# Kernel optimization log

Measured on AMD Instinct MI355X. Metric: run time of the kernel, lower is better.

The kernel has to match this reference:

```python
import jax, jax.numpy as jnp
import numpy as np

K = 2  # shift stride from module init


def setup_inputs() -> dict:
    key = jax.random.key(0)
    k1, k2, k3 = jax.random.split(key, 3)
    # x: [B, C, D, H, W] dense volumetric features
    x = jax.random.normal(k1, (2, 128, 48, 48, 48), dtype=jnp.float32)
    # 1x1x1 Conv3d weight [out_channels, 2*in_channels] (kernel dims squeezed) + bias
    W = jax.random.normal(k2, (128, 256), dtype=jnp.float32) * 0.02
    b = jax.random.normal(k3, (128,), dtype=jnp.float32) * 0.02
    return {"x": x, "W": W, "b": b}


def _max_relative(x):
    # torch.cat([x[..., -i:], x[..., :-i]], dim=ax) == roll by +i along ax
    B, C, D, H, Wd = x.shape
    xj = jnp.zeros_like(x)  # x - x
    for axis, n in ((2, D), (3, H), (4, Wd)):
        for i in range(K, n, K):  # static shift schedule, fine under jit
            xj = jnp.maximum(xj, x - jnp.roll(x, i, axis=axis))
    return xj


def reference(x, W, b):
    xj = _max_relative(x)
    y = jnp.concatenate([x, xj], axis=1)  # [B, 2C, D, H, W]
    # 1x1x1 conv == channel GEMM
    out = jnp.einsum('bcdhw,oc->bodhw', y, W) + b[None, :, None, None, None]
    return jax.nn.relu(out)
```

## Files before the change

kernel.cpp:

```cpp
#include <hip/hip_runtime.h>
#include <hip/hip_bf16.h>

#define SVOL 110592
#define HD   2304
#define NDIM 48

typedef __attribute__((ext_vector_type(4))) float f32x4;
typedef __attribute__((ext_vector_type(8))) short bf16x8;
typedef __attribute__((ext_vector_type(2))) unsigned int u32x2;
typedef unsigned short ushort_t;
typedef unsigned int uint_t;

__global__ __launch_bounds__(256) void wconv_kernel(const float* __restrict__ W,
                                                    ushort_t* __restrict__ Wb) {
    int i = blockIdx.x * 256 + threadIdx.x;
    float f = W[i];
    __hip_bfloat16 h = __float2bfloat16(f);
    Wb[i] = *(ushort_t*)&h;
}

__global__ __launch_bounds__(256) void tables_kernel(const float* __restrict__ x,
                                                     float* __restrict__ tabDp,
                                                     float* __restrict__ tabH,
                                                     float* __restrict__ tabW) {
    __shared__ __align__(16) float sl[4 * HD];
    const int bc   = blockIdx.x;
    const int part = blockIdx.y;
    const float* __restrict__ xp = x + (size_t)bc * SVOL + (size_t)part * 16 * HD;
    const int t    = threadIdx.x;
    const int w4   = t >> 6;
    const int lane = t & 63;
    const int dlh  = t / NDIM;
    const int wh   = t - dlh * NDIM;

    f32x4 accD[3][2];
    #pragma unroll
    for (int s = 0; s < 3; ++s)
        #pragma unroll
        for (int p = 0; p < 2; ++p)
            #pragma unroll
            for (int e = 0; e < 4; ++e) accD[s][p][e] = 3e38f;

    for (int q = 0; q < 4; ++q) {
        const float* __restrict__ qp = xp + (size_t)q * 4 * HD;
        #pragma unroll
        for (int k = 0; k < 9; ++k) {
            const int i16 = (k * 4 + w4) * 64 + lane;
            __builtin_amdgcn_global_load_lds(
                (const __attribute__((address_space(1))) void*)(qp + (size_t)i16 * 4),
                (__attribute__((address_space(3))) void*)&sl[(k * 4 + w4) * 256],
                16, 0, 0);
        }
        __syncthreads();

        #pragma unroll
        for (int s = 0; s < 3; ++s) {
            const int j = t + s * 256;
            if (j < 576) {
                #pragma unroll
                for (int dl = 0; dl < 4; ++dl) {
                    f32x4 v = ((const f32x4*)sl)[dl * 576 + j];
                    #pragma unroll
                    for (int e = 0; e < 4; ++e)
                        accD[s][dl & 1][e] = fminf(accD[s][dl & 1][e], v[e]);
                }
            }
        }
        if (t < 192) {
            const int d = part * 16 + q * 4 + dlh;
            {
                const float* pb = sl + dlh * HD + wh;
                float m0 = 3e38f, m1 = 3e38f;
                #pragma unroll
                for (int h = 0; h < NDIM; h += 2) {
                    m0 = fminf(m0, pb[h * NDIM]);
                    m1 = fminf(m1, pb[(h + 1) * NDIM]);
                }
                tabH[(size_t)bc * 2 * HD + d * NDIM + wh]      = m0;
                tabH[(size_t)bc * 2 * HD + HD + d * NDIM + wh] = m1;
            }
            {
                const f32x4* pr = (const f32x4*)(sl + dlh * HD + wh * NDIM);
                const int rot = wh % 12;
                float m0 = 3e38f, m1 = 3e38f;
                #pragma unroll
                for (int j = 0; j < 12; ++j) {
                    int jj = j + rot; if (jj >= 12) jj -= 12;
                    f32x4 v = pr[jj];
                    m0 = fminf(m0, fminf(v[0], v[2]));
                    m1 = fminf(m1, fminf(v[1], v[3]));
                }
                tabW[(size_t)bc * 2 * HD + d * NDIM + wh]      = m0;
                tabW[(size_t)bc * 2 * HD + HD + d * NDIM + wh] = m1;
            }
        }
        __syncthreads();
    }

    float* tDo = tabDp + ((size_t)part * 256 + bc) * 2 * HD;
    #pragma unroll
    for (int s = 0; s < 3; ++s) {
        const int j = t + s * 256;
        if (j < 576) {
            *((f32x4*)(tDo + j * 4))      = accD[s][0];
            *((f32x4*)(tDo + HD + j * 4)) = accD[s][1];
        }
    }
}

__global__ __launch_bounds__(256) void merge_kernel(const float* __restrict__ tabDp,
                                                    float* __restrict__ tabD) {
    const int i = blockIdx.x * 256 + threadIdx.x;
    f32x4 a  = ((const f32x4*)tabDp)[i];
    f32x4 d1 = ((const f32x4*)(tabDp + (size_t)256 * 2 * HD))[i];
    f32x4 d2 = ((const f32x4*)(tabDp + (size_t)2 * 256 * 2 * HD))[i];
    f32x4 m;
    #pragma unroll
    for (int j = 0; j < 4; ++j) m[j] = fminf(a[j], fminf(d1[j], d2[j]));
    ((f32x4*)tabD)[i] = m;
}

#define TPB 4
__global__ __launch_bounds__(256, 2) void gemm_kernel(const float* __restrict__ x,
                                                      const float* __restrict__ tabD,
                                                      const float* __restrict__ tabH,
                                                      const float* __restrict__ tabW,
                                                      const ushort_t* __restrict__ Wb,
                                                      const float* __restrict__ bias,
                                                      float* __restrict__ out) {
    __shared__ __align__(1024) ushort_t ytile[16384];
    const int tile0 = blockIdx.x * TPB;
    const int b  = blockIdx.y;
    const int t  = threadIdx.x;
    const int wid = t >> 6, lane = t & 63;
    const int row  = lane & 3;
    const int colq = (lane >> 2) & 3;
    const int sqq  = (lane >> 4) & 3;
    const int sloc = (sqq * 4 + colq) * 4;
    const int l15 = lane & 15, l4 = lane >> 4;

    const float* __restrict__ xb = x + (size_t)b * 128 * SVOL;
    const size_t tbb = (size_t)b * 128 * 2 * HD;

    const ushort_t* wp = Wb + (size_t)(wid * 32 + l15) * 256 + l4 * 8;
    float bv[2];
    #pragma unroll
    for (int m = 0; m < 2; ++m) bv[m] = bias[wid * 32 + m * 16 + l15];

    const int d  = (tile0 * 64) / HD;
    const int rb = tile0 * 64 - d * HD;
    const int pd = d & 1;

    uint2 pk[8][2];
    auto stage = [&](int tile) {
        const int r  = rb + (tile - tile0) * 64 + sloc;
        const int h  = r / NDIM;
        const int w0 = r - h * NDIM;
        const int ph = h & 1;
        const int s  = d * HD + r;
        #pragma unroll
        for (int it = 0; it < 8; ++it) {
            const int c = (it * 4 + wid) * 4 + row;
            const size_t tb = tbb + (size_t)c * 2 * HD;
            f32x4 xv = *(const f32x4*)(xb + (size_t)c * SVOL + s);
            f32x4 mD = *(const f32x4*)(tabD + tb + pd * HD + r);
            f32x4 mH = *(const f32x4*)(tabH + tb + ph * HD + d * NDIM + w0);
            const float mW0 = tabW[tb + d * NDIM + h];
            const float mW1 = tabW[tb + HD + d * NDIM + h];
            union { __hip_bfloat16 h4[4]; uint2 u; } ox, oj;
            #pragma unroll
            for (int j = 0; j < 4; ++j) {
                const float mm = fminf(mD[j], fminf(mH[j], (j & 1) ? mW1 : mW0));
                ox.h4[j] = __float2bfloat16(xv[j]);
                oj.h4[j] = __float2bfloat16(fmaxf(0.0f, xv[j] - mm));
            }
            pk[it][0] = ox.u; pk[it][1] = oj.u;
        }
    };

    const uint_t lds_base = (uint_t)(uintptr_t)(__attribute__((address_space(3))) ushort_t*)&ytile[0];
    float* ob = out + (size_t)b * 128 * SVOL;

    stage(tile0);

    #pragma unroll
    for (int tt = 0; tt < TPB; ++tt) {
        __syncthreads();
        {
            #pragma unroll
            for (int it = 0; it < 8; ++it) {
                const int A = (it * 4 + wid) * 512 + sqq * 128 + row * 32 + colq * 8;
                *(uint2*)&ytile[A >> 1]             = pk[it][0];
                *(uint2*)&ytile[(A + 16384) >> 1]   = pk[it][1];
            }
        }
        __syncthreads();

        const uint_t addrB = lds_base + (uint_t)(l4 * 1024 + l15 * 8);
        f32x4 acc[4][2] = {};
        #pragma unroll
        for (int ph2 = 0; ph2 < 2; ++ph2) {
            u32x2 lo[4][4], hi[4][4];
            #pragma unroll
            for (int kk = 0; kk < 4; ++kk)
                #pragma unroll
                for (int n = 0; n < 4; ++n) {
                    const uint_t ad = addrB + (uint_t)((ph2 * 4 + kk) * 4096 + n * 128);
                    asm volatile("ds_read_b64_tr_b16 %0, %2 offset:0\n\t"
                                 "ds_read_b64_tr_b16 %1, %2 offset:512"
                                 : "=&v"(lo[kk][n]), "=&v"(hi[kk][n]) : "v"(ad) : "memory");
                }
            asm volatile("s_waitcnt lgkmcnt(0)" ::: "memory");
            __builtin_amdgcn_sched_barrier(0);
            #pragma unroll
            for (int kk = 0; kk < 4; ++kk) {
                bf16x8 aw[2];
                #pragma unroll
                for (int m = 0; m < 2; ++m)
                    aw[m] = *(const bf16x8*)(wp + ((size_t)m * 16 * 256 + (ph2 * 4 + kk) * 32));
                #pragma unroll
                for (int n = 0; n < 4; ++n) {
                    union { u32x2 u2[2]; bf16x8 v; } cvt;
                    cvt.u2[0] = lo[kk][n]; cvt.u2[1] = hi[kk][n];
                    #pragma unroll
                    for (int m = 0; m < 2; ++m)
                        acc[n][m] = __builtin_amdgcn_mfma_f32_16x16x32_bf16(cvt.v, aw[m], acc[n][m], 0, 0, 0);
                }
            }
        }

        if (tt + 1 < TPB) stage(tile0 + tt + 1);

        const int s_b = (tile0 + tt) * 64;
        #pragma unroll
        for (int n = 0; n < 4; ++n)
            #pragma unroll
            for (int m = 0; m < 2; ++m) {
                const int o = wid * 32 + m * 16 + l15;
                const int s = s_b + n * 16 + l4 * 4;
                f32x4 r;
                #pragma unroll
                for (int j = 0; j < 4; ++j) r[j] = fmaxf(acc[n][m][j] + bv[m], 0.0f);
                *(f32x4*)(ob + (size_t)o * SVOL + s) = r;
            }
    }
}

extern "C" void kernel_launch(void* const* d_in, const int* in_sizes, int n_in,
                              void* d_out, int out_size, void* d_ws, size_t ws_size,
                              hipStream_t stream) {
    const float* x    = (const float*)d_in[0];
    const float* W    = (const float*)d_in[1];
    const float* bias = (const float*)d_in[2];
    float* out = (float*)d_out;

    ushort_t* Wb   = (ushort_t*)d_ws;
    float* tabDp = (float*)((char*)d_ws + 65536);
    float* tabH  = tabDp + (size_t)3 * 256 * 2 * HD;
    float* tabW  = tabH  + (size_t)256 * 2 * HD;
    float* tabD  = tabW  + (size_t)256 * 2 * HD;

    wconv_kernel<<<128, 256, 0, stream>>>(W, Wb);
    tables_kernel<<<dim3(256, 3), 256, 0, stream>>>(x, tabDp, tabH, tabW);
    merge_kernel<<<1152, 256, 0, stream>>>(tabDp, tabD);
    gemm_kernel<<<dim3(SVOL / 64 / TPB, 2), 256, 0, stream>>>(x, tabD, tabH, tabW, Wb, bias, out);
}
```

Baseline: 135.8 us.

## Split fused GEMM into elementwise fragment prepack kernel and direct-load MFMA GEMM

```diff
diff --git a/kernel.cpp b/kernel.cpp
--- a/kernel.cpp
+++ b/kernel.cpp
@@ -7,7 +7,6 @@
 
 typedef __attribute__((ext_vector_type(4))) float f32x4;
 typedef __attribute__((ext_vector_type(8))) short bf16x8;
-typedef __attribute__((ext_vector_type(2))) unsigned int u32x2;
 typedef unsigned short ushort_t;
 typedef unsigned int uint_t;
 
@@ -120,130 +119,91 @@
     ((f32x4*)tabD)[i] = m;
 }
 
-#define TPB 4
-__global__ __launch_bounds__(256, 2) void gemm_kernel(const float* __restrict__ x,
-                                                      const float* __restrict__ tabD,
-                                                      const float* __restrict__ tabH,
-                                                      const float* __restrict__ tabW,
-                                                      const ushort_t* __restrict__ Wb,
-                                                      const float* __restrict__ bias,
-                                                      float* __restrict__ out) {
-    __shared__ __align__(1024) ushort_t ytile[16384];
-    const int tile0 = blockIdx.x * TPB;
+__global__ __launch_bounds__(256) void elem_frag_kernel(const float* __restrict__ x,
+                                                        const float* __restrict__ tabD,
+                                                        const float* __restrict__ tabH,
+                                                        const float* __restrict__ tabW,
+                                                        ushort_t* __restrict__ yfrag) {
+    const int t   = threadIdx.x;
+    const int s   = blockIdx.x * 256 + t;
+    const int bco = blockIdx.y;
+    const int b   = bco >> 4, co = bco & 15;
+    const int c8  = co * 8;
+
+    const int d = s / HD, r = s - d * HD;
+    const int h = r / NDIM, w = r - h * NDIM;
+    const int pd = d & 1, ph = h & 1, pw = w & 1;
+
+    const size_t dhw = (size_t)d * NDIM;
+    union { ushort_t u8[8]; uint4 v; } px, pj;
+    #pragma unroll
+    for (int j = 0; j < 8; ++j) {
+        const int c = c8 + j;
+        const size_t tb = (size_t)(b * 128 + c) * 2 * HD;
+        const float xv = x[(size_t)(b * 128 + c) * SVOL + s];
+        const float mD = tabD[tb + (size_t)pd * HD + r];
+        const float mH = tabH[tb + (size_t)ph * HD + dhw + w];
+        const float mW = tabW[tb + (size_t)pw * HD + dhw + h];
+        const float mm = fminf(mD, fminf(mH, mW));
+        __hip_bfloat16 hx = __float2bfloat16(xv);
+        __hip_bfloat16 hj = __float2bfloat16(fmaxf(0.0f, xv - mm));
+        px.u8[j] = *(ushort_t*)&hx;
+        pj.u8[j] = *(ushort_t*)&hj;
+    }
+
+    const int kk = co >> 2, l4 = co & 3;
+    const size_t ux = (((size_t)(b * 6912 + (s >> 4))) * 8 + kk) * 512
+                    + (size_t)(l4 * 16 + (s & 15)) * 8;
+    *(uint4*)&yfrag[ux]        = px.v;
+    *(uint4*)&yfrag[ux + 2048] = pj.v;
+}
+
+__global__ __launch_bounds__(256) void gemm_direct_kernel(const ushort_t* __restrict__ yfrag,
+                                                          const ushort_t* __restrict__ Wb,
+                                                          const float* __restrict__ bias,
+                                                          float* __restrict__ out) {
+    const int bx = blockIdx.x;
     const int b  = blockIdx.y;
     const int t  = threadIdx.x;
     const int wid = t >> 6, lane = t & 63;
-    const int row  = lane & 3;
-    const int colq = (lane >> 2) & 3;
-    const int sqq  = (lane >> 4) & 3;
-    const int sloc = (sqq * 4 + colq) * 4;
     const int l15 = lane & 15, l4 = lane >> 4;
-
-    const float* __restrict__ xb = x + (size_t)b * 128 * SVOL;
-    const size_t tbb = (size_t)b * 128 * 2 * HD;
-
-    const ushort_t* wp = Wb + (size_t)(wid * 32 + l15) * 256 + l4 * 8;
-    float bv[2];
-    #pragma unroll
-    for (int m = 0; m < 2; ++m) bv[m] = bias[wid * 32 + m * 16 + l15];
-
-    const int d  = (tile0 * 64) / HD;
-    const int rb = tile0 * 64 - d * HD;
-    const int pd = d & 1;
-
-    uint2 pk[8][2];
-    auto stage = [&](int tile) {
-        const int r  = rb + (tile - tile0) * 64 + sloc;
-        const int h  = r / NDIM;
-        const int w0 = r - h * NDIM;
-        const int ph = h & 1;
-        const int s  = d * HD + r;
-        #pragma unroll
-        for (int it = 0; it < 8; ++it) {
-            const int c = (it * 4 + wid) * 4 + row;
-            const size_t tb = tbb + (size_t)c * 2 * HD;
-            f32x4 xv = *(const f32x4*)(xb + (size_t)c * SVOL + s);
-            f32x4 mD = *(const f32x4*)(tabD + tb + pd * HD + r);
-            f32x4 mH = *(const f32x4*)(tabH + tb + ph * HD + d * NDIM + w0);
-            const float mW0 = tabW[tb + d * NDIM + h];
-            const float mW1 = tabW[tb + HD + d * NDIM + h];
-            union { __hip_bfloat16 h4[4]; uint2 u; } ox, oj;
-            #pragma unroll
-            for (int j = 0; j < 4; ++j) {
-                const float mm = fminf(mD[j], fminf(mH[j], (j & 1) ? mW1 : mW0));
-                ox.h4[j] = __float2bfloat16(xv[j]);
-                oj.h4[j] = __float2bfloat16(fmaxf(0.0f, xv[j] - mm));
-            }
-            pk[it][0] = ox.u; pk[it][1] = oj.u;
-        }
-    };
-
-    const uint_t lds_base = (uint_t)(uintptr_t)(__attribute__((address_space(3))) ushort_t*)&ytile[0];
-    float* ob = out + (size_t)b * 128 * SVOL;
-
-    stage(tile0);
-
-    #pragma unroll
-    for (int tt = 0; tt < TPB; ++tt) {
-        __syncthreads();
-        {
-            #pragma unroll
-            for (int it = 0; it < 8; ++it) {
-                const int A = (it * 4 + wid) * 512 + sqq * 128 + row * 32 + colq * 8;
-                *(uint2*)&ytile[A >> 1]             = pk[it][0];
-                *(uint2*)&ytile[(A + 16384) >> 1]   = pk[it][1];
-            }
-        }
-        __syncthreads();
-
-        const uint_t addrB = lds_base + (uint_t)(l4 * 1024 + l15 * 8);
-        f32x4 acc[4][2] = {};
-        #pragma unroll
-        for (int ph2 = 0; ph2 < 2; ++ph2) {
-            u32x2 lo[4][4], hi[4][4];
-            #pragma unroll
-            for (int kk = 0; kk < 4; ++kk)
-                #pragma unroll
-                for (int n = 0; n < 4; ++n) {
-                    const uint_t ad = addrB + (uint_t)((ph2 * 4 + kk) * 4096 + n * 128);
-                    asm volatile("ds_read_b64_tr_b16 %0, %2 offset:0\n\t"
-                                 "ds_read_b64_tr_b16 %1, %2 offset:512"
-                                 : "=&v"(lo[kk][n]), "=&v"(hi[kk][n]) : "v"(ad) : "memory");
-                }
-            asm volatile("s_waitcnt lgkmcnt(0)" ::: "memory");
-            __builtin_amdgcn_sched_barrier(0);
-            #pragma unroll
-            for (int kk = 0; kk < 4; ++kk) {
-                bf16x8 aw[2];
-                #pragma unroll
-                for (int m = 0; m < 2; ++m)
-                    aw[m] = *(const bf16x8*)(wp + ((size_t)m * 16 * 256 + (ph2 * 4 + kk) * 32));
-                #pragma unroll
-                for (int n = 0; n < 4; ++n) {
-                    union { u32x2 u2[2]; bf16x8 v; } cvt;
-                    cvt.u2[0] = lo[kk][n]; cvt.u2[1] = hi[kk][n];
-                    #pragma unroll
-                    for (int m = 0; m < 2; ++m)
-                        acc[n][m] = __builtin_amdgcn_mfma_f32_16x16x32_bf16(cvt.v, aw[m], acc[n][m], 0, 0, 0);
-                }
-            }
-        }
-
-        if (tt + 1 < TPB) stage(tile0 + tt + 1);
-
-        const int s_b = (tile0 + tt) * 64;
+    const int s0 = bx * 64, st0 = s0 >> 4;
+
+    const ushort_t* __restrict__ yb = yfrag + (size_t)b * 6912 * 8 * 512;
+    const ushort_t* __restrict__ wp = Wb + (size_t)(wid * 32 + l15) * 256 + l4 * 8;
+
+    f32x4 acc[4][2] = {};
+    #pragma unroll
+    for (int kk = 0; kk < 8; ++kk) {
+        bf16x8 a[4], aw[2];
+        #pragma unroll
+        for (int n = 0; n < 4; ++n)
+            a[n] = *(const bf16x8*)(yb + ((size_t)(st0 + n) * 8 + kk) * 512 + lane * 8);
+        #pragma unroll
+        for (int m = 0; m < 2; ++m)
+            aw[m] = *(const bf16x8*)(wp + (size_t)m * 16 * 256 + kk * 32);
         #pragma unroll
         for (int n = 0; n < 4; ++n)
             #pragma unroll
-            for (int m = 0; m < 2; ++m) {
-                const int o = wid * 32 + m * 16 + l15;
-                const int s = s_b + n * 16 + l4 * 4;
-                f32x4 r;
-                #pragma unroll
-                for (int j = 0; j < 4; ++j) r[j] = fmaxf(acc[n][m][j] + bv[m], 0.0f);
-                *(f32x4*)(ob + (size_t)o * SVOL + s) = r;
-            }
-    }
+            for (int m = 0; m < 2; ++m)
+                acc[n][m] = __builtin_amdgcn_mfma_f32_16x16x32_bf16(a[n], aw[m], acc[n][m], 0, 0, 0);
+    }
+
+    float bv[2];
+    bv[0] = bias[wid * 32 + l15];
+    bv[1] = bias[wid * 32 + 16 + l15];
+    float* ob = out + (size_t)b * 128 * SVOL;
+    #pragma unroll
+    for (int n = 0; n < 4; ++n)
+        #pragma unroll
+        for (int m = 0; m < 2; ++m) {
+            const int o = wid * 32 + m * 16 + l15;
+            const int s = s0 + n * 16 + l4 * 4;
+            f32x4 r;
+            #pragma unroll
+            for (int j = 0; j < 4; ++j) r[j] = fmaxf(acc[n][m][j] + bv[m], 0.0f);
+            *(f32x4*)(ob + (size_t)o * SVOL + s) = r;
+        }
 }
 
 extern "C" void kernel_launch(void* const* d_in, const int* in_sizes, int n_in,
@@ -254,8 +214,10 @@
     const float* bias = (const float*)d_in[2];
     float* out = (float*)d_out;
 
-    ushort_t* Wb   = (ushort_t*)d_ws;
-    float* tabDp = (float*)((char*)d_ws + 65536);
+    ushort_t* yfrag = (ushort_t*)d_ws;
+    ushort_t* Wb    = (ushort_t*)((char*)d_ws + (size_t)2 * 256 * SVOL * 2);
+
+    float* tabDp = (float*)d_out;
     float* tabH  = tabDp + (size_t)3 * 256 * 2 * HD;
     float* tabW  = tabH  + (size_t)256 * 2 * HD;
     float* tabD  = tabW  + (size_t)256 * 2 * HD;
@@ -263,5 +225,6 @@
     wconv_kernel<<<128, 256, 0, stream>>>(W, Wb);
     tables_kernel<<<dim3(256, 3), 256, 0, stream>>>(x, tabDp, tabH, tabW);
     merge_kernel<<<1152, 256, 0, stream>>>(tabDp, tabD);
-    gemm_kernel<<<dim3(SVOL / 64 / TPB, 2), 256, 0, stream>>>(x, tabD, tabH, tabW, Wb, bias, out);
-}
+    elem_frag_kernel<<<dim3(432, 32), 256, 0, stream>>>(x, tabD, tabH, tabW, yfrag);
+    gemm_direct_kernel<<<dim3(SVOL / 64, 2), 256, 0, stream>>>(yfrag, Wb, bias, out);
+}
```

Result: slower. 151.1 us (+11.2%).
